# Kernel tuning notes

Hardware: AMD Instinct MI355X
Metric: run time of the kernel (lower is better)

## Reference

```python
import jax, jax.numpy as jnp
import numpy as np

N_NODES = 100000
N_EDGES = 3200000
IN_SIZE = 128
HID = 128
OUT = 64
HEADS = (4, 1)
NEG_SLOPE = 0.2  # DGL GATConv default leaky_relu slope


def setup_inputs() -> dict:
    key = jax.random.key(0)
    ks = jax.random.split(key, 10)
    x = jax.random.normal(ks[0], (N_NODES, IN_SIZE), dtype=jnp.float32)
    src = jax.random.randint(ks[1], (N_EDGES,), 0, N_NODES, dtype=jnp.int64)
    dst = jax.random.randint(ks[2], (N_EDGES,), 0, N_NODES, dtype=jnp.int64)
    s1 = 1.0 / np.sqrt(IN_SIZE)
    s2 = 1.0 / np.sqrt(HID * HEADS[0])
    W1 = jax.random.normal(ks[3], (IN_SIZE, HEADS[0] * HID), dtype=jnp.float32) * s1
    al1 = jax.random.normal(ks[4], (HEADS[0], HID), dtype=jnp.float32) * 0.1
    ar1 = jax.random.normal(ks[5], (HEADS[0], HID), dtype=jnp.float32) * 0.1
    W2 = jax.random.normal(ks[6], (HEADS[0] * HID, HEADS[1] * OUT), dtype=jnp.float32) * s2
    al2 = jax.random.normal(ks[7], (HEADS[1], OUT), dtype=jnp.float32) * 0.1
    ar2 = jax.random.normal(ks[8], (HEADS[1], OUT), dtype=jnp.float32) * 0.1
    return {"x": x, "W1": W1, "al1": al1, "ar1": ar1, "W2": W2,
            "al2": al2, "ar2": ar2, "src": src, "dst": dst}


def gat_conv(h, W, al, ar, src, dst, n_heads, d_out):
    # h: (N, F_in); W: (F_in, n_heads*d_out); al/ar: (n_heads, d_out)
    n = h.shape[0]
    feat = (h @ W).reshape(n, n_heads, d_out)          # (N, H, D)
    el = jnp.sum(feat * al, axis=-1)                    # (N, H) source score
    er = jnp.sum(feat * ar, axis=-1)                    # (N, H) dest score
    e = jax.nn.leaky_relu(el[src] + er[dst], NEG_SLOPE)  # (E, H)
    # edge softmax over incoming edges of each destination node
    m = jax.ops.segment_max(e, dst, num_segments=n)     # (N, H)
    m = jnp.where(jnp.isfinite(m), m, 0.0)              # nodes with no in-edges
    ex = jnp.exp(e - m[dst])                            # (E, H)
    s = jax.ops.segment_sum(ex, dst, num_segments=n)    # (N, H)
    alpha = ex / s[dst]                                 # (E, H); s[dst]>0 always
    msg = alpha[:, :, None] * feat[src]                 # (E, H, D)
    out = jax.ops.segment_sum(msg, dst, num_segments=n)  # (N, H, D)
    return out


def reference(x, W1, al1, ar1, W2, al2, ar2, src, dst):
    n = x.shape[0]
    h = gat_conv(x, W1, al1, ar1, src, dst, HEADS[0], HID)   # (N, H1, HID)
    h = jax.nn.elu(h).reshape(n, HEADS[0] * HID)             # flatten(1)
    h = gat_conv(h, W2, al2, ar2, src, dst, HEADS[1], OUT)   # (N, H2, OUT)
    h = h.reshape(n * HEADS[1], OUT)                          # view(N*H2, OUT)
    return h
```

## Files before the change

kernel.cpp:

```cpp
#include <hip/hip_runtime.h>
#include <math.h>

#define N_NODES 100000
#define N_EDGES 3200000
#define NEG 0.2f
#define NPB 128
#define NB  782
#define CAP 4608
#define LOG2E 1.442695041f

typedef __attribute__((ext_vector_type(8))) short short8;
typedef __attribute__((ext_vector_type(4))) float f32x4;
typedef __attribute__((ext_vector_type(2))) float f32x2;

__device__ __forceinline__ float bflo(unsigned int u){
  union { unsigned int i; float f; } v; v.i = u << 16; return v.f;
}
__device__ __forceinline__ float bfhi(unsigned int u){
  union { unsigned int i; float f; } v; v.i = u & 0xffff0000u; return v.f;
}
__device__ __forceinline__ unsigned short f2bf(float f){
  union { float f; unsigned int i; } v; v.f = f;
  unsigned int r = v.i + 0x7fffu + ((v.i >> 16) & 1u);
  return (unsigned short)(r >> 16);
}
__device__ __forceinline__ unsigned int packbf(float lo, float hi){
  return (unsigned int)f2bf(lo) | ((unsigned int)f2bf(hi) << 16);
}
__device__ __forceinline__ unsigned int pk_fp8x4(float a, float b, float c, float d){
  int v = 0;
  v = __builtin_amdgcn_cvt_pk_fp8_f32(a, b, v, false);
  v = __builtin_amdgcn_cvt_pk_fp8_f32(c, d, v, true);
  return (unsigned int)v;
}
__device__ __forceinline__ f32x2 unpk_fp8_lo(unsigned int v){
  return __builtin_amdgcn_cvt_pk_f32_fp8((int)v, false);
}
__device__ __forceinline__ f32x2 unpk_fp8_hi(unsigned int v){
  return __builtin_amdgcn_cvt_pk_f32_fp8((int)v, true);
}
__device__ __forceinline__ void pk_fma(f32x2 &acc, f32x2 a, f32x2 w){
  asm("v_pk_fma_f32 %0, %1, %2, %0" : "+v"(acc) : "v"(a), "v"(w));
}
__device__ __forceinline__ float wexp(float t){
  return __builtin_amdgcn_exp2f(fmaxf(t, NEG * t));
}
__device__ __forceinline__ void fma16(f32x2* acc, uint4 q, float w){
  f32x2 W; W[0]=w; W[1]=w;
  pk_fma(acc[0], unpk_fp8_lo(q.x), W);
  pk_fma(acc[1], unpk_fp8_hi(q.x), W);
  pk_fma(acc[2], unpk_fp8_lo(q.y), W);
  pk_fma(acc[3], unpk_fp8_hi(q.y), W);
  pk_fma(acc[4], unpk_fp8_lo(q.z), W);
  pk_fma(acc[5], unpk_fp8_hi(q.z), W);
  pk_fma(acc[6], unpk_fp8_lo(q.w), W);
  pk_fma(acc[7], unpk_fp8_hi(q.w), W);
}

__global__ void k_prep(const float* __restrict__ W1, const float* __restrict__ W2,
                       unsigned short* __restrict__ W1t, unsigned short* __restrict__ W2t,
                       int* __restrict__ bcur){
  int i = blockIdx.x*256 + threadIdx.x;
  if (i < 65536){ int n = i >> 7, k = i & 127; W1t[i] = f2bf(W1[k*512 + n]); }
  else if (i < 98304){ int j = i - 65536; int n = j >> 9, k = j & 511; W2t[j] = f2bf(W2[k*64 + n]); }
  else if (i < 98304 + NB){ int b = i - 98304; bcur[b*16] = b*CAP; }
}

__global__ __launch_bounds__(256) void k_mm1(const float* __restrict__ A,
    const unsigned short* __restrict__ Bt,
    unsigned char* __restrict__ C8, int M,
    const float* __restrict__ al, const float* __restrict__ ar,
    float* __restrict__ el, float* __restrict__ er){
  __shared__ unsigned short sm[18432];
  unsigned short* As = sm;
  unsigned short* Bs = sm + 9216;
  const int t = threadIdx.x;
  const int w = t >> 6, l = t & 63;
  const int quad = l >> 4, l16 = l & 15;
  const int m0 = blockIdx.x * 128;
  const int head = blockIdx.y;
  const int moff = (w & 1) * 64, noff = (w >> 1) * 64;
  f32x4 acc[4][4];
  #pragma unroll
  for (int i=0;i<4;++i)
    #pragma unroll
    for (int j=0;j<4;++j){ acc[i][j][0]=0.f; acc[i][j][1]=0.f; acc[i][j][2]=0.f; acc[i][j][3]=0.f; }
  for (int kb = 0; kb < 2; ++kb){
    const int K0 = kb * 64;
    #pragma unroll
    for (int i=0;i<8;++i){
      int idx = t + i*256;
      int row = idx >> 4, c4 = (idx & 15) * 4;
      float4 v = make_float4(0.f,0.f,0.f,0.f);
      if (m0 + row < M) v = *(const float4*)(A + (size_t)(m0+row)*128 + K0 + c4);
      uint2 p; p.x = packbf(v.x, v.y); p.y = packbf(v.z, v.w);
      *(uint2*)(As + row*72 + c4) = p;
    }
    #pragma unroll
    for (int i=0;i<4;++i){
      int idx = t + i*256;
      int row = idx >> 3, c8 = (idx & 7) * 8;
      *(uint4*)(Bs + row*72 + c8) =
        *(const uint4*)(Bt + (size_t)(head*128 + row)*128 + K0 + c8);
    }
    __syncthreads();
    #pragma unroll
    for (int ks = 0; ks < 2; ++ks){
      short8 af[4], bfr[4];
      #pragma unroll
      for (int mi=0; mi<4; ++mi)
        af[mi] = *(const short8*)(As + (moff + mi*16 + l16)*72 + ks*32 + quad*8);
      #pragma unroll
      for (int ni=0; ni<4; ++ni)
        bfr[ni] = *(const short8*)(Bs + (noff + ni*16 + l16)*72 + ks*32 + quad*8);
      #pragma unroll
      for (int mi=0; mi<4; ++mi)
        #pragma unroll
        for (int ni=0; ni<4; ++ni)
          acc[mi][ni] = __builtin_amdgcn_mfma_f32_16x16x32_bf16(af[mi], bfr[ni], acc[mi][ni], 0,0,0);
    }
    __syncthreads();
  }
  unsigned short* Cs = sm;
  #pragma unroll
  for (int mi=0; mi<4; ++mi)
    #pragma unroll
    for (int ni=0; ni<4; ++ni){
      int col = noff + ni*16 + l16;
      int rb  = moff + mi*16 + quad*4;
      #pragma unroll
      for (int r=0;r<4;++r) Cs[(rb+r)*136 + col] = f2bf(acc[mi][ni][r]);
    }
  __syncthreads();
  const int hcol = head * 128;
  #pragma unroll
  for (int i=0;i<8;++i){
    int e = t + i*256;
    int row = e >> 4, c8 = (e & 15) * 8;
    uint4 qb = *(const uint4*)(Cs + row*136 + c8);
    uint2 o;
    o.x = pk_fp8x4(bflo(qb.x), bfhi(qb.x), bflo(qb.y), bfhi(qb.y));
    o.y = pk_fp8x4(bflo(qb.z), bfhi(qb.z), bflo(qb.w), bfhi(qb.w));
    if (m0 + row < M)
      *(uint2*)(C8 + (size_t)(m0+row)*512 + hcol + c8) = o;
  }
  {
    int row = t >> 1, half = t & 1;
    const float* alp = al + head*128 + half*64;
    const float* arp = ar + head*128 + half*64;
    const unsigned short* cp = Cs + row*136 + half*64;
    float se = 0.f, sr = 0.f;
    #pragma unroll
    for (int i=0;i<8;++i){
      uint4 q = *(const uint4*)(cp + i*8);
      float4 a0 = *(const float4*)(alp + i*8), a1 = *(const float4*)(alp + i*8 + 4);
      float4 r0 = *(const float4*)(arp + i*8), r1 = *(const float4*)(arp + i*8 + 4);
      se += bflo(q.x)*a0.x + bfhi(q.x)*a0.y + bflo(q.y)*a0.z + bfhi(q.y)*a0.w
          + bflo(q.z)*a1.x + bfhi(q.z)*a1.y + bflo(q.w)*a1.z + bfhi(q.w)*a1.w;
      sr += bflo(q.x)*r0.x + bfhi(q.x)*r0.y + bflo(q.y)*r0.z + bfhi(q.y)*r0.w
          + bflo(q.z)*r1.x + bfhi(q.z)*r1.y + bflo(q.w)*r1.z + bfhi(q.w)*r1.w;
    }
    se += __shfl_xor(se, 1); sr += __shfl_xor(sr, 1);
    if (half == 0 && m0 + row < M){
      el[(m0+row)*4 + head] = se * LOG2E;
      er[(m0+row)*4 + head] = sr * LOG2E;
    }
  }
}

__global__ __launch_bounds__(256) void k_mm2(const unsigned short* __restrict__ A,
    const unsigned short* __restrict__ Bt,
    unsigned short* __restrict__ C, int M,
    const float* __restrict__ al, const float* __restrict__ ar,
    float* __restrict__ el, float* __restrict__ er){
  __shared__ unsigned short sm[13824];
  unsigned short* As = sm;
  unsigned short* Bs = sm + 9216;
  const int t = threadIdx.x;
  const int w = t >> 6, l = t & 63;
  const int quad = l >> 4, l16 = l & 15;
  const int m0 = blockIdx.x * 128;
  const int moff = w * 32;
  f32x4 acc[2][4];
  #pragma unroll
  for (int i=0;i<2;++i)
    #pragma unroll
    for (int j=0;j<4;++j){ acc[i][j][0]=0.f; acc[i][j][1]=0.f; acc[i][j][2]=0.f; acc[i][j][3]=0.f; }
  for (int kb = 0; kb < 8; ++kb){
    const int K0 = kb * 64;
    #pragma unroll
    for (int i=0;i<4;++i){
      int idx = t + i*256;
      int row = idx >> 3, c8 = (idx & 7) * 8;
      uint4 v; v.x=0u; v.y=0u; v.z=0u; v.w=0u;
      if (m0 + row < M) v = *(const uint4*)(A + (size_t)(m0+row)*512 + K0 + c8);
      *(uint4*)(As + row*72 + c8) = v;
    }
    #pragma unroll
    for (int i=0;i<2;++i){
      int idx = t + i*256;
      int row = idx >> 3, c8 = (idx & 7) * 8;
      *(uint4*)(Bs + row*72 + c8) = *(const uint4*)(Bt + (size_t)row*512 + K0 + c8);
    }
    __syncthreads();
    #pragma unroll
    for (int ks = 0; ks < 2; ++ks){
      short8 af[2], bfr[4];
      #pragma unroll
      for (int mi=0; mi<2; ++mi)
        af[mi] = *(const short8*)(As + (moff + mi*16 + l16)*72 + ks*32 + quad*8);
      #pragma unroll
      for (int ni=0; ni<4; ++ni)
        bfr[ni] = *(const short8*)(Bs + (ni*16 + l16)*72 + ks*32 + quad*8);
      #pragma unroll
      for (int mi=0; mi<2; ++mi)
        #pragma unroll
        for (int ni=0; ni<4; ++ni)
          acc[mi][ni] = __builtin_amdgcn_mfma_f32_16x16x32_bf16(af[mi], bfr[ni], acc[mi][ni], 0,0,0);
    }
    __syncthreads();
  }
  unsigned short* Cs = sm;
  #pragma unroll
  for (int mi=0; mi<2; ++mi)
    #pragma unroll
    for (int ni=0; ni<4; ++ni){
      int col = ni*16 + l16;
      int rb  = moff + mi*16 + quad*4;
      #pragma unroll
      for (int r=0;r<4;++r) Cs[(rb+r)*72 + col] = f2bf(acc[mi][ni][r]);
    }
  __syncthreads();
  #pragma unroll
  for (int i=0;i<4;++i){
    int e = t + i*256;
    int row = e >> 3, c8 = (e & 7) * 8;
    if (m0 + row < M)
      *(uint4*)(C + (size_t)(m0+row)*64 + c8) = *(const uint4*)(Cs + row*72 + c8);
  }
  {
    int row = t >> 1, half = t & 1;
    const float* alp = al + half*32;
    const float* arp = ar + half*32;
    const unsigned short* cp = Cs + row*72 + half*32;
    float se = 0.f, sr = 0.f;
    #pragma unroll
    for (int i=0;i<4;++i){
      uint4 q = *(const uint4*)(cp + i*8);
      float4 a0 = *(const float4*)(alp + i*8), a1 = *(const float4*)(alp + i*8 + 4);
      float4 r0 = *(const float4*)(arp + i*8), r1 = *(const float4*)(arp + i*8 + 4);
      se += bflo(q.x)*a0.x + bfhi(q.x)*a0.y + bflo(q.y)*a0.z + bfhi(q.y)*a0.w
          + bflo(q.z)*a1.x + bfhi(q.z)*a1.y + bflo(q.w)*a1.z + bfhi(q.w)*a1.w;
      sr += bflo(q.x)*r0.x + bfhi(q.x)*r0.y + bflo(q.y)*r0.z + bfhi(q.y)*r0.w
          + bflo(q.z)*r1.x + bfhi(q.z)*r1.y + bflo(q.w)*r1.z + bfhi(q.w)*r1.w;
    }
    se += __shfl_xor(se, 1); sr += __shfl_xor(sr, 1);
    if (half == 0 && m0 + row < M){
      el[m0+row] = se * LOG2E;
      er[m0+row] = sr * LOG2E;
    }
  }
}

__global__ void k_bucket(const int* __restrict__ src, const int* __restrict__ dst,
                         int* __restrict__ bcur, int* __restrict__ staged){
  int e = blockIdx.x*blockDim.x + threadIdx.x;
  if (e < N_EDGES){
    int d = dst[e];
    int b = d >> 7;
    int pos = atomicAdd(&bcur[b*16], 1);
    staged[pos] = (src[e] << 7) | (d & (NPB-1));
  }
}
__global__ __launch_bounds__(1024) void k_bscan(const int* __restrict__ bcur,
    int* __restrict__ bbase){
  __shared__ int lds[1024];
  int t = threadIdx.x;
  int v = (t < NB) ? (bcur[t*16] - t*CAP) : 0;
  lds[t] = v; __syncthreads();
  for (int off=1; off<1024; off<<=1){
    int u = (t>=off)? lds[t-off] : 0;
    __syncthreads();
    lds[t] += u;
    __syncthreads();
  }
  if (t < NB) bbase[t] = lds[t] - v;
  if (t == 0) bbase[NB] = N_EDGES;
}
__global__ __launch_bounds__(256) void k_binsort(const int* __restrict__ staged,
    const int* __restrict__ bcur, const int* __restrict__ bbase,
    int* __restrict__ csr_src, int* __restrict__ indptr){
  __shared__ int hist[NPB];
  __shared__ int scan[NPB];
  __shared__ int lcur[NPB];
  const int b = blockIdx.x, t = threadIdx.x;
  const int st0 = b*CAP;
  const int cnt = bcur[b*16] - st0;
  const int obase = bbase[b];
  if (t < NPB) hist[t] = 0;
  __syncthreads();
  for (int i = t; i < cnt; i += 256)
    atomicAdd(&hist[staged[st0 + i] & (NPB-1)], 1);
  __syncthreads();
  int v = (t < NPB) ? hist[t] : 0;
  if (t < NPB) scan[t] = v;
  __syncthreads();
  for (int off=1; off<NPB; off<<=1){
    int u = (t < NPB && t >= off) ? scan[t-off] : 0;
    __syncthreads();
    if (t < NPB) scan[t] += u;
    __syncthreads();
  }
  const int node0 = b * NPB;
  if (t < NPB){
    int ex = obase + scan[t] - v;
    lcur[t] = ex;
    if (node0 + t < N_NODES) indptr[node0 + t] = ex;
  }
  if (b == NB-1 && t == 0) indptr[N_NODES] = N_EDGES;
  __syncthreads();
  for (int i = t; i < cnt; i += 256){
    int pv = staged[st0 + i];
    int pos = atomicAdd(&lcur[pv & (NPB-1)], 1);
    csr_src[pos] = pv >> 7;
  }
}

__global__ __launch_bounds__(256) void k_agg1(const unsigned char* __restrict__ feat,
    const float* __restrict__ el, const float* __restrict__ er,
    const int* __restrict__ indptr, const int* __restrict__ csr_src,
    unsigned short* __restrict__ out){
  int wave = threadIdx.x >> 6, lane = threadIdx.x & 63;
  int n = blockIdx.x*4 + wave;
  if (n >= N_NODES) return;
  int p0 = indptr[n], p1 = indptr[n+1];
  const int half = lane >> 5, hl = lane & 31;
  const int hh = hl >> 3;
  const unsigned d0 = hl * 16u;
  const float myer = er[n*4 + hh];
  float ssum = 0.f;
  f32x2 acc[8];
  #pragma unroll
  for (int i=0;i<8;++i){ acc[i][0]=0.f; acc[i][1]=0.f; }
  int e = p0;
  for (; e + 7 < p1; e += 8){
    int s0 = csr_src[e + 0 + half];
    int s1 = csr_src[e + 2 + half];
    int s2 = csr_src[e + 4 + half];
    int s3 = csr_src[e + 6 + half];
    uint4 q0 = *(const uint4*)(feat + (((unsigned)s0) << 9) + d0);
    uint4 q1 = *(const uint4*)(feat + (((unsigned)s1) << 9) + d0);
    uint4 q2 = *(const uint4*)(feat + (((unsigned)s2) << 9) + d0);
    uint4 q3 = *(const uint4*)(feat + (((unsigned)s3) << 9) + d0);
    float t0 = el[(s0<<2) + hh] + myer;
    float t1 = el[(s1<<2) + hh] + myer;
    float t2 = el[(s2<<2) + hh] + myer;
    float t3 = el[(s3<<2) + hh] + myer;
    float w0 = wexp(t0), w1 = wexp(t1), w2 = wexp(t2), w3 = wexp(t3);
    ssum += (w0 + w1) + (w2 + w3);
    fma16(acc, q0, w0);
    fma16(acc, q1, w1);
    fma16(acc, q2, w2);
    fma16(acc, q3, w3);
  }
  for (; e < p1; e += 2){
    int idx = e + half;
    bool ok = idx < p1;
    int s = csr_src[ok ? idx : e];
    uint4 q = *(const uint4*)(feat + (((unsigned)s) << 9) + d0);
    float w = ok ? wexp(el[(s<<2) + hh] + myer) : 0.f;
    ssum += w;
    fma16(acc, q, w);
  }
  ssum += __shfl_xor(ssum, 32);
  float o16[16];
  #pragma unroll
  for (int i=0;i<8;++i){
    o16[2*i]   = acc[i][0] + __shfl_xor(acc[i][0], 32);
    o16[2*i+1] = acc[i][1] + __shfl_xor(acc[i][1], 32);
  }
  float inv = ssum > 0.f ? 1.f/ssum : 0.f;
  #pragma unroll
  for (int i=0;i<16;++i){
    float v = o16[i] * inv;
    o16[i] = v > 0.f ? v : __expf(v) - 1.f;
  }
  if (half == 0){
    unsigned short* op = out + (size_t)n*512 + hl*16;
    uint4 oa, ob;
    oa.x = packbf(o16[0], o16[1]);  oa.y = packbf(o16[2], o16[3]);
    oa.z = packbf(o16[4], o16[5]);  oa.w = packbf(o16[6], o16[7]);
    ob.x = packbf(o16[8], o16[9]);  ob.y = packbf(o16[10],o16[11]);
    ob.z = packbf(o16[12],o16[13]); ob.w = packbf(o16[14],o16[15]);
    *(uint4*)op       = oa;
    *(uint4*)(op + 8) = ob;
  }
}

__global__ __launch_bounds__(256) void k_agg2(const unsigned short* __restrict__ feat,
    const float* __restrict__ el, const float* __restrict__ er,
    const int* __restrict__ indptr, const int* __restrict__ csr_src,
    float* __restrict__ out){
  int wave = threadIdx.x >> 6, lane = threadIdx.x & 63;
  int n = blockIdx.x*4 + wave;
  if (n >= N_NODES) return;
  int p0 = indptr[n], p1 = indptr[n+1];
  float ern = er[n];
  int g = lane >> 3, ql = lane & 7;
  float s = 0.f;
  f32x2 acc[4];
  #pragma unroll
  for (int i=0;i<4;++i){ acc[i][0]=0.f; acc[i][1]=0.f; }
  int e = p0 + g;
  for (; e + 8 < p1; e += 16){
    int sa = csr_src[e], sb = csr_src[e+8];
    uint4 va = *(const uint4*)(feat + (size_t)sa*64 + ql*8);
    uint4 vb = *(const uint4*)(feat + (size_t)sb*64 + ql*8);
    float wa = wexp(el[sa] + ern);
    float wb = wexp(el[sb] + ern);
    s += wa + wb;
    f32x2 Wa; Wa[0]=wa; Wa[1]=wa;
    f32x2 Wb; Wb[0]=wb; Wb[1]=wb;
    f32x2 a;
    a[0]=bflo(va.x); a[1]=bfhi(va.x); pk_fma(acc[0], a, Wa);
    a[0]=bflo(va.y); a[1]=bfhi(va.y); pk_fma(acc[1], a, Wa);
    a[0]=bflo(va.z); a[1]=bfhi(va.z); pk_fma(acc[2], a, Wa);
    a[0]=bflo(va.w); a[1]=bfhi(va.w); pk_fma(acc[3], a, Wa);
    a[0]=bflo(vb.x); a[1]=bfhi(vb.x); pk_fma(acc[0], a, Wb);
// ... 19 lines not shown
    #pragma unroll
    for (int i=0;i<4;++i){
      acc[i][0] += __shfl_xor(acc[i][0],m);
      acc[i][1] += __shfl_xor(acc[i][1],m);
    }
  }
  float inv = s > 0.f ? 1.f/s : 0.f;
  if (g == 0){
    float* op = out + (size_t)n*64 + ql*8;
    *(float4*)op     = make_float4(acc[0][0]*inv, acc[0][1]*inv, acc[1][0]*inv, acc[1][1]*inv);
    *(float4*)(op+4) = make_float4(acc[2][0]*inv, acc[2][1]*inv, acc[3][0]*inv, acc[3][1]*inv);
  }
}

extern "C" void kernel_launch(void* const* d_in, const int* in_sizes, int n_in,
                              void* d_out, int out_size, void* d_ws, size_t ws_size,
                              hipStream_t stream){
  const float* x   = (const float*)d_in[0];
  const float* W1  = (const float*)d_in[1];
  const float* al1 = (const float*)d_in[2];
  const float* ar1 = (const float*)d_in[3];
  const float* W2  = (const float*)d_in[4];
  const float* al2 = (const float*)d_in[5];
  const float* ar2 = (const float*)d_in[6];
  const int* src   = (const int*)d_in[7];
  const int* dst   = (const int*)d_in[8];
  float* out = (float*)d_out;

  char* ws = (char*)d_ws;
  size_t off = 0;
  auto alloc = [&](size_t bytes)->char*{
    char* p = ws + off; off += (bytes + 255) & ~(size_t)255; return p;
  };
  unsigned char*  feat1 = (unsigned char*)alloc((size_t)N_NODES*512);
  unsigned short* h1    = (unsigned short*)alloc((size_t)N_NODES*512*2);
  unsigned short* feat2b = (unsigned short*)feat1;
  unsigned short* W1t = (unsigned short*)alloc(512*128*2);
  unsigned short* W2t = (unsigned short*)alloc(64*512*2);
  float* el1 = (float*)alloc((size_t)N_NODES*4*4);
  float* er1 = (float*)alloc((size_t)N_NODES*4*4);
  float* el2 = el1;
  float* er2 = er1;
  int* bcur    = (int*)alloc((size_t)NB*16*4);
  int* bbase   = (int*)alloc((size_t)(NB+1)*4);
  int* indptr  = (int*)alloc((size_t)(N_NODES+1)*4);
  int* staged  = (int*)alloc((size_t)NB*CAP*4);
  int* csr_src = (int*)alloc((size_t)N_EDGES*4);

  dim3 b256(256);
  k_prep<<<dim3(388), b256, 0, stream>>>(W1, W2, W1t, W2t, bcur);
  k_mm1<<<dim3(782, 4), b256, 0, stream>>>(x, W1t, feat1, N_NODES, al1, ar1, el1, er1);
  k_bucket<<<dim3((N_EDGES+255)/256), b256, 0, stream>>>(src, dst, bcur, staged);
  k_bscan<<<dim3(1), dim3(1024), 0, stream>>>(bcur, bbase);
  k_binsort<<<dim3(NB), b256, 0, stream>>>(staged, bcur, bbase, csr_src, indptr);
  k_agg1<<<dim3(25000), b256, 0, stream>>>(feat1, el1, er1, indptr, csr_src, h1);
  k_mm2<<<dim3(782), b256, 0, stream>>>(h1, W2t, feat2b, N_NODES, al2, ar2, el2, er2);
  k_agg2<<<dim3(25000), b256, 0, stream>>>(feat2b, el2, er2, indptr, csr_src, out);
}
```

Measured before the change: 724.4 us.

## Fuse GEMM1 with edge bucketing and binsort into two heterogeneous kernels

Merges the first-layer projection GEMM with the edge bucketing pass in one kernel (heads 0-1 interleaved with bucket blocks), then runs heads 2-3 alongside the per-bucket sort in a second kernel. The compute-bound GEMM blocks are meant to overlap the memory and atomic-bound CSR build, and removing the single-block scan kernel cuts launches. Each binsort block now recomputes its output base by summing all preceding bucket counts. The fat kernels reserve the larger shared-memory footprint for every block, which can lower occupancy for the bucketing blocks.

```diff
diff --git a/kernel.cpp b/kernel.cpp
--- a/kernel.cpp
+++ b/kernel.cpp
@@ -66,19 +66,18 @@
   else if (i < 98304 + NB){ int b = i - 98304; bcur[b*16] = b*CAP; }
 }
 
-__global__ __launch_bounds__(256) void k_mm1(const float* __restrict__ A,
-    const unsigned short* __restrict__ Bt,
+__device__ void mm1_body(char* smraw, int mtile, int head,
+    const float* __restrict__ A, const unsigned short* __restrict__ Bt,
     unsigned char* __restrict__ C8, int M,
     const float* __restrict__ al, const float* __restrict__ ar,
     float* __restrict__ el, float* __restrict__ er){
-  __shared__ unsigned short sm[18432];
+  unsigned short* sm = (unsigned short*)smraw;
   unsigned short* As = sm;
   unsigned short* Bs = sm + 9216;
   const int t = threadIdx.x;
   const int w = t >> 6, l = t & 63;
   const int quad = l >> 4, l16 = l & 15;
-  const int m0 = blockIdx.x * 128;
-  const int head = blockIdx.y;
+  const int m0 = mtile * 128;
   const int moff = (w & 1) * 64, noff = (w >> 1) * 64;
   f32x4 acc[4][4];
   #pragma unroll
@@ -165,6 +164,99 @@
       el[(m0+row)*4 + head] = se * LOG2E;
       er[(m0+row)*4 + head] = sr * LOG2E;
     }
+  }
+}
+
+__device__ void bucket_body(int eb, const int* __restrict__ src,
+    const int* __restrict__ dst, int* __restrict__ bcur, int* __restrict__ staged){
+  int e = eb*256 + threadIdx.x;
+  if (e < N_EDGES){
+    int d = dst[e];
+    int b = d >> 7;
+    int pos = atomicAdd(&bcur[b*16], 1);
+    staged[pos] = (src[e] << 7) | (d & (NPB-1));
+  }
+}
+
+__device__ void binsort_body(char* smraw, int b, const int* __restrict__ staged,
+    const int* __restrict__ bcur, int* __restrict__ csr_src, int* __restrict__ indptr){
+  int* hist = (int*)smraw;
+  int* scan = hist + 128;
+  int* lcur = scan + 128;
+  int* red  = lcur + 128;
+  const int t = threadIdx.x;
+  const int st0 = b*CAP;
+  const int cnt = bcur[b*16] - st0;
+  int part = 0;
+  for (int i = t; i < b; i += 256) part += bcur[i*16] - i*CAP;
+  red[t] = part;
+  if (t < NPB) hist[t] = 0;
+  __syncthreads();
+  for (int off = 128; off > 0; off >>= 1){
+    if (t < off) red[t] += red[t + off];
+    __syncthreads();
+  }
+  const int obase = red[0];
+  for (int i = t; i < cnt; i += 256)
+    atomicAdd(&hist[staged[st0 + i] & (NPB-1)], 1);
+  __syncthreads();
+  int v = (t < NPB) ? hist[t] : 0;
+  if (t < NPB) scan[t] = v;
+  __syncthreads();
+  for (int off=1; off<NPB; off<<=1){
+    int u = (t < NPB && t >= off) ? scan[t-off] : 0;
+    __syncthreads();
+    if (t < NPB) scan[t] += u;
+    __syncthreads();
+  }
+  const int node0 = b * NPB;
+  if (t < NPB){
+    int ex = obase + scan[t] - v;
+    lcur[t] = ex;
+    if (node0 + t < N_NODES) indptr[node0 + t] = ex;
+  }
+  if (b == NB-1 && t == 0) indptr[N_NODES] = N_EDGES;
+  __syncthreads();
+  for (int i = t; i < cnt; i += 256){
+    int pv = staged[st0 + i];
+    int pos = atomicAdd(&lcur[pv & (NPB-1)], 1);
+    csr_src[pos] = pv >> 7;
+  }
+}
+
+__global__ __launch_bounds__(256) void k_fatA(const float* __restrict__ x,
+    const unsigned short* __restrict__ W1t, unsigned char* __restrict__ feat1,
+    const float* __restrict__ al1, const float* __restrict__ ar1,
+    float* __restrict__ el1, float* __restrict__ er1,
+    const int* __restrict__ src, const int* __restrict__ dst,
+    int* __restrict__ bcur, int* __restrict__ staged){
+  __shared__ char smraw[36864];
+  int b = blockIdx.x;
+  int r = b % 9;
+  if (r == 0){
+    int id = b / 9;
+    mm1_body(smraw, id % 782, id / 782, x, W1t, feat1, N_NODES, al1, ar1, el1, er1);
+  } else {
+    int id = (b/9)*8 + (r-1);
+    if (id < 12500) bucket_body(id, src, dst, bcur, staged);
+  }
+}
+
+__global__ __launch_bounds__(256) void k_fatB(const float* __restrict__ x,
+    const unsigned short* __restrict__ W1t, unsigned char* __restrict__ feat1,
+    const float* __restrict__ al1, const float* __restrict__ ar1,
+    float* __restrict__ el1, float* __restrict__ er1,
+    const int* __restrict__ staged, const int* __restrict__ bcur,
+    int* __restrict__ csr_src, int* __restrict__ indptr){
+  __shared__ char smraw[36864];
+  int b = blockIdx.x;
+  int r = b % 3;
+  if (r < 2){
+    int id = (b/3)*2 + r;
+    mm1_body(smraw, id % 782, 2 + id / 782, x, W1t, feat1, N_NODES, al1, ar1, el1, er1);
+  } else {
+    int id = b / 3;
+    binsort_body(smraw, id, staged, bcur, csr_src, indptr);
   }
 }
 
@@ -259,70 +351,6 @@
       el[m0+row] = se * LOG2E;
       er[m0+row] = sr * LOG2E;
     }
-  }
-}
-
-__global__ void k_bucket(const int* __restrict__ src, const int* __restrict__ dst,
-                         int* __restrict__ bcur, int* __restrict__ staged){
-  int e = blockIdx.x*blockDim.x + threadIdx.x;
-  if (e < N_EDGES){
-    int d = dst[e];
-    int b = d >> 7;
-    int pos = atomicAdd(&bcur[b*16], 1);
-    staged[pos] = (src[e] << 7) | (d & (NPB-1));
-  }
-}
-__global__ __launch_bounds__(1024) void k_bscan(const int* __restrict__ bcur,
-    int* __restrict__ bbase){
-  __shared__ int lds[1024];
-  int t = threadIdx.x;
-  int v = (t < NB) ? (bcur[t*16] - t*CAP) : 0;
-  lds[t] = v; __syncthreads();
-  for (int off=1; off<1024; off<<=1){
-    int u = (t>=off)? lds[t-off] : 0;
-    __syncthreads();
-    lds[t] += u;
-    __syncthreads();
-  }
-  if (t < NB) bbase[t] = lds[t] - v;
-  if (t == 0) bbase[NB] = N_EDGES;
-}
-__global__ __launch_bounds__(256) void k_binsort(const int* __restrict__ staged,
-    const int* __restrict__ bcur, const int* __restrict__ bbase,
-    int* __restrict__ csr_src, int* __restrict__ indptr){
-  __shared__ int hist[NPB];
-  __shared__ int scan[NPB];
-  __shared__ int lcur[NPB];
-  const int b = blockIdx.x, t = threadIdx.x;
-  const int st0 = b*CAP;
-  const int cnt = bcur[b*16] - st0;
-  const int obase = bbase[b];
-  if (t < NPB) hist[t] = 0;
-  __syncthreads();
-  for (int i = t; i < cnt; i += 256)
-    atomicAdd(&hist[staged[st0 + i] & (NPB-1)], 1);
-  __syncthreads();
-  int v = (t < NPB) ? hist[t] : 0;
-  if (t < NPB) scan[t] = v;
-  __syncthreads();
-  for (int off=1; off<NPB; off<<=1){
-    int u = (t < NPB && t >= off) ? scan[t-off] : 0;
-    __syncthreads();
-    if (t < NPB) scan[t] += u;
-    __syncthreads();
-  }
-  const int node0 = b * NPB;
-  if (t < NPB){
-    int ex = obase + scan[t] - v;
-    lcur[t] = ex;
-    if (node0 + t < N_NODES) indptr[node0 + t] = ex;
-  }
-  if (b == NB-1 && t == 0) indptr[N_NODES] = N_EDGES;
-  __syncthreads();
-  for (int i = t; i < cnt; i += 256){
-    int pv = staged[st0 + i];
-    int pos = atomicAdd(&lcur[pv & (NPB-1)], 1);
-    csr_src[pos] = pv >> 7;
   }
 }
 
@@ -489,17 +517,16 @@
   float* el2 = el1;
   float* er2 = er1;
   int* bcur    = (int*)alloc((size_t)NB*16*4);
-  int* bbase   = (int*)alloc((size_t)(NB+1)*4);
   int* indptr  = (int*)alloc((size_t)(N_NODES+1)*4);
   int* staged  = (int*)alloc((size_t)NB*CAP*4);
   int* csr_src = (int*)alloc((size_t)N_EDGES*4);
 
   dim3 b256(256);
   k_prep<<<dim3(388), b256, 0, stream>>>(W1, W2, W1t, W2t, bcur);
-  k_mm1<<<dim3(782, 4), b256, 0, stream>>>(x, W1t, feat1, N_NODES, al1, ar1, el1, er1);
-  k_bucket<<<dim3((N_EDGES+255)/256), b256, 0, stream>>>(src, dst, bcur, staged);
-  k_bscan<<<dim3(1), dim3(1024), 0, stream>>>(bcur, bbase);
-  k_binsort<<<dim3(NB), b256, 0, stream>>>(staged, bcur, bbase, csr_src, indptr);
+  k_fatA<<<dim3(14076), b256, 0, stream>>>(x, W1t, feat1, al1, ar1, el1, er1,
+                                           src, dst, bcur, staged);
+  k_fatB<<<dim3(2346), b256, 0, stream>>>(x, W1t, feat1, al1, ar1, el1, er1,
+                                          staged, bcur, csr_src, indptr);
   k_agg1<<<dim3(25000), b256, 0, stream>>>(feat1, el1, er1, indptr, csr_src, h1);
   k_mm2<<<dim3(782), b256, 0, stream>>>(h1, W2t, feat2b, N_NODES, al2, ar2, el2, er2);
   k_agg2<<<dim3(25000), b256, 0, stream>>>(feat2b, el2, er2, indptr, csr_src, out);
```

After: 780.4 us. 7.7% more time.

## Aggregate raw input features before layer-1 projection, folding attention vectors into W1

Applied to the files above, without the earlier changes.

Layer 1 now gathers neighbours' 128-wide bf16 input rows instead of 512-wide fp8 projected features. The projection by W1 moves after aggregation, with the softmax normalisation and ELU applied in a new GEMM epilogue. Attention scores are computed directly from x using W1·al and W1·ar precomputed in the prep kernel. This cuts per-edge gather bytes and drops the fp8 quantisation, at the cost of a separate conversion pass, an extra bf16 intermediate round-trip, and doing the 4-head weighted accumulation per edge in registers.

```diff
diff --git a/kernel.cpp b/kernel.cpp
--- a/kernel.cpp
+++ b/kernel.cpp
@@ -27,238 +27,92 @@
 __device__ __forceinline__ unsigned int packbf(float lo, float hi){
   return (unsigned int)f2bf(lo) | ((unsigned int)f2bf(hi) << 16);
 }
-__device__ __forceinline__ unsigned int pk_fp8x4(float a, float b, float c, float d){
-  int v = 0;
-  v = __builtin_amdgcn_cvt_pk_fp8_f32(a, b, v, false);
-  v = __builtin_amdgcn_cvt_pk_fp8_f32(c, d, v, true);
-  return (unsigned int)v;
-}
-__device__ __forceinline__ f32x2 unpk_fp8_lo(unsigned int v){
-  return __builtin_amdgcn_cvt_pk_f32_fp8((int)v, false);
-}
-__device__ __forceinline__ f32x2 unpk_fp8_hi(unsigned int v){
-  return __builtin_amdgcn_cvt_pk_f32_fp8((int)v, true);
-}
 __device__ __forceinline__ void pk_fma(f32x2 &acc, f32x2 a, f32x2 w){
   asm("v_pk_fma_f32 %0, %1, %2, %0" : "+v"(acc) : "v"(a), "v"(w));
 }
 __device__ __forceinline__ float wexp(float t){
   return __builtin_amdgcn_exp2f(fmaxf(t, NEG * t));
 }
-__device__ __forceinline__ void fma16(f32x2* acc, uint4 q, float w){
-  f32x2 W; W[0]=w; W[1]=w;
-  pk_fma(acc[0], unpk_fp8_lo(q.x), W);
-  pk_fma(acc[1], unpk_fp8_hi(q.x), W);
-  pk_fma(acc[2], unpk_fp8_lo(q.y), W);
-  pk_fma(acc[3], unpk_fp8_hi(q.y), W);
-  pk_fma(acc[4], unpk_fp8_lo(q.z), W);
-  pk_fma(acc[5], unpk_fp8_hi(q.z), W);
-  pk_fma(acc[6], unpk_fp8_lo(q.w), W);
-  pk_fma(acc[7], unpk_fp8_hi(q.w), W);
+__device__ __forceinline__ f32x4 wexp4(f32x4 t){
+  f32x4 r; r[0]=wexp(t[0]); r[1]=wexp(t[1]); r[2]=wexp(t[2]); r[3]=wexp(t[3]);
+  return r;
+}
+__device__ __forceinline__ void fma_x8(f32x2 (*acc)[4], uint4 q, f32x4 w){
+  f32x2 p0,p1,p2,p3;
+  p0[0]=bflo(q.x); p0[1]=bfhi(q.x);
+  p1[0]=bflo(q.y); p1[1]=bfhi(q.y);
+  p2[0]=bflo(q.z); p2[1]=bfhi(q.z);
+  p3[0]=bflo(q.w); p3[1]=bfhi(q.w);
+  #pragma unroll
+  for (int h=0;h<4;++h){
+    f32x2 W; W[0]=w[h]; W[1]=w[h];
+    pk_fma(acc[h][0], p0, W);
+    pk_fma(acc[h][1], p1, W);
+    pk_fma(acc[h][2], p2, W);
+    pk_fma(acc[h][3], p3, W);
+  }
 }
 
 __global__ void k_prep(const float* __restrict__ W1, const float* __restrict__ W2,
+                       const float* __restrict__ al1, const float* __restrict__ ar1,
                        unsigned short* __restrict__ W1t, unsigned short* __restrict__ W2t,
-                       int* __restrict__ bcur){
+                       int* __restrict__ bcur, float* __restrict__ val,
+                       float* __restrict__ var){
   int i = blockIdx.x*256 + threadIdx.x;
   if (i < 65536){ int n = i >> 7, k = i & 127; W1t[i] = f2bf(W1[k*512 + n]); }
   else if (i < 98304){ int j = i - 65536; int n = j >> 9, k = j & 511; W2t[j] = f2bf(W2[k*64 + n]); }
   else if (i < 98304 + NB){ int b = i - 98304; bcur[b*16] = b*CAP; }
-}
-
-__global__ __launch_bounds__(256) void k_mm1(const float* __restrict__ A,
-    const unsigned short* __restrict__ Bt,
-    unsigned char* __restrict__ C8, int M,
-    const float* __restrict__ al, const float* __restrict__ ar,
-    float* __restrict__ el, float* __restrict__ er){
-  __shared__ unsigned short sm[18432];
-  unsigned short* As = sm;
-  unsigned short* Bs = sm + 9216;
-  const int t = threadIdx.x;
-  const int w = t >> 6, l = t & 63;
-  const int quad = l >> 4, l16 = l & 15;
-  const int m0 = blockIdx.x * 128;
-  const int head = blockIdx.y;
-  const int moff = (w & 1) * 64, noff = (w >> 1) * 64;
-  f32x4 acc[4][4];
-  #pragma unroll
-  for (int i=0;i<4;++i)
-    #pragma unroll
-    for (int j=0;j<4;++j){ acc[i][j][0]=0.f; acc[i][j][1]=0.f; acc[i][j][2]=0.f; acc[i][j][3]=0.f; }
-  for (int kb = 0; kb < 2; ++kb){
-    const int K0 = kb * 64;
-    #pragma unroll
-    for (int i=0;i<8;++i){
-      int idx = t + i*256;
-      int row = idx >> 4, c4 = (idx & 15) * 4;
-      float4 v = make_float4(0.f,0.f,0.f,0.f);
-      if (m0 + row < M) v = *(const float4*)(A + (size_t)(m0+row)*128 + K0 + c4);
-      uint2 p; p.x = packbf(v.x, v.y); p.y = packbf(v.z, v.w);
-      *(uint2*)(As + row*72 + c4) = p;
-    }
-    #pragma unroll
-    for (int i=0;i<4;++i){
-      int idx = t + i*256;
-      int row = idx >> 3, c8 = (idx & 7) * 8;
-      *(uint4*)(Bs + row*72 + c8) =
-        *(const uint4*)(Bt + (size_t)(head*128 + row)*128 + K0 + c8);
-    }
-    __syncthreads();
-    #pragma unroll
-    for (int ks = 0; ks < 2; ++ks){
-      short8 af[4], bfr[4];
-      #pragma unroll
-      for (int mi=0; mi<4; ++mi)
-        af[mi] = *(const short8*)(As + (moff + mi*16 + l16)*72 + ks*32 + quad*8);
-      #pragma unroll
-      for (int ni=0; ni<4; ++ni)
-        bfr[ni] = *(const short8*)(Bs + (noff + ni*16 + l16)*72 + ks*32 + quad*8);
-      #pragma unroll
-      for (int mi=0; mi<4; ++mi)
-        #pragma unroll
-        for (int ni=0; ni<4; ++ni)
-          acc[mi][ni] = __builtin_amdgcn_mfma_f32_16x16x32_bf16(af[mi], bfr[ni], acc[mi][ni], 0,0,0);
-    }
-    __syncthreads();
-  }
-  unsigned short* Cs = sm;
-  #pragma unroll
-  for (int mi=0; mi<4; ++mi)
-    #pragma unroll
-    for (int ni=0; ni<4; ++ni){
-      int col = noff + ni*16 + l16;
-      int rb  = moff + mi*16 + quad*4;
-      #pragma unroll
-      for (int r=0;r<4;++r) Cs[(rb+r)*136 + col] = f2bf(acc[mi][ni][r]);
-    }
-  __syncthreads();
-  const int hcol = head * 128;
-  #pragma unroll
-  for (int i=0;i<8;++i){
-    int e = t + i*256;
-    int row = e >> 4, c8 = (e & 15) * 8;
-    uint4 qb = *(const uint4*)(Cs + row*136 + c8);
-    uint2 o;
-    o.x = pk_fp8x4(bflo(qb.x), bfhi(qb.x), bflo(qb.y), bfhi(qb.y));
-    o.y = pk_fp8x4(bflo(qb.z), bfhi(qb.z), bflo(qb.w), bfhi(qb.w));
-    if (m0 + row < M)
-      *(uint2*)(C8 + (size_t)(m0+row)*512 + hcol + c8) = o;
-  }
-  {
-    int row = t >> 1, half = t & 1;
-    const float* alp = al + head*128 + half*64;
-    const float* arp = ar + head*128 + half*64;
-    const unsigned short* cp = Cs + row*136 + half*64;
-    float se = 0.f, sr = 0.f;
-    #pragma unroll
-    for (int i=0;i<8;++i){
-      uint4 q = *(const uint4*)(cp + i*8);
-      float4 a0 = *(const float4*)(alp + i*8), a1 = *(const float4*)(alp + i*8 + 4);
-      float4 r0 = *(const float4*)(arp + i*8), r1 = *(const float4*)(arp + i*8 + 4);
-      se += bflo(q.x)*a0.x + bfhi(q.x)*a0.y + bflo(q.y)*a0.z + bfhi(q.y)*a0.w
-          + bflo(q.z)*a1.x + bfhi(q.z)*a1.y + bflo(q.w)*a1.z + bfhi(q.w)*a1.w;
-      sr += bflo(q.x)*r0.x + bfhi(q.x)*r0.y + bflo(q.y)*r0.z + bfhi(q.y)*r0.w
-          + bflo(q.z)*r1.x + bfhi(q.z)*r1.y + bflo(q.w)*r1.z + bfhi(q.w)*r1.w;
-    }
-    se += __shfl_xor(se, 1); sr += __shfl_xor(sr, 1);
-    if (half == 0 && m0 + row < M){
-      el[(m0+row)*4 + head] = se * LOG2E;
-      er[(m0+row)*4 + head] = sr * LOG2E;
-    }
-  }
-}
-
-__global__ __launch_bounds__(256) void k_mm2(const unsigned short* __restrict__ A,
-    const unsigned short* __restrict__ Bt,
-    unsigned short* __restrict__ C, int M,
-    const float* __restrict__ al, const float* __restrict__ ar,
-    float* __restrict__ el, float* __restrict__ er){
-  __shared__ unsigned short sm[13824];
-  unsigned short* As = sm;
-  unsigned short* Bs = sm + 9216;
-  const int t = threadIdx.x;
-  const int w = t >> 6, l = t & 63;
-  const int quad = l >> 4, l16 = l & 15;
-  const int m0 = blockIdx.x * 128;
-  const int moff = w * 32;
-  f32x4 acc[2][4];
-  #pragma unroll
-  for (int i=0;i<2;++i)
-    #pragma unroll
-    for (int j=0;j<4;++j){ acc[i][j][0]=0.f; acc[i][j][1]=0.f; acc[i][j][2]=0.f; acc[i][j][3]=0.f; }
-  for (int kb = 0; kb < 8; ++kb){
-    const int K0 = kb * 64;
-    #pragma unroll
-    for (int i=0;i<4;++i){
-      int idx = t + i*256;
-      int row = idx >> 3, c8 = (idx & 7) * 8;
-      uint4 v; v.x=0u; v.y=0u; v.z=0u; v.w=0u;
-      if (m0 + row < M) v = *(const uint4*)(A + (size_t)(m0+row)*512 + K0 + c8);
-      *(uint4*)(As + row*72 + c8) = v;
-    }
-    #pragma unroll
-    for (int i=0;i<2;++i){
-      int idx = t + i*256;
-      int row = idx >> 3, c8 = (idx & 7) * 8;
-      *(uint4*)(Bs + row*72 + c8) = *(const uint4*)(Bt + (size_t)row*512 + K0 + c8);
-    }
-    __syncthreads();
-    #pragma unroll
-    for (int ks = 0; ks < 2; ++ks){
-      short8 af[2], bfr[4];
-      #pragma unroll
-      for (int mi=0; mi<2; ++mi)
-        af[mi] = *(const short8*)(As + (moff + mi*16 + l16)*72 + ks*32 + quad*8);
-      #pragma unroll
-      for (int ni=0; ni<4; ++ni)
-        bfr[ni] = *(const short8*)(Bs + (ni*16 + l16)*72 + ks*32 + quad*8);
-      #pragma unroll
-      for (int mi=0; mi<2; ++mi)
-        #pragma unroll
-        for (int ni=0; ni<4; ++ni)
-          acc[mi][ni] = __builtin_amdgcn_mfma_f32_16x16x32_bf16(af[mi], bfr[ni], acc[mi][ni], 0,0,0);
-    }
-    __syncthreads();
-  }
-  unsigned short* Cs = sm;
-  #pragma unroll
-  for (int mi=0; mi<2; ++mi)
-    #pragma unroll
-    for (int ni=0; ni<4; ++ni){
-      int col = ni*16 + l16;
-      int rb  = moff + mi*16 + quad*4;
-      #pragma unroll
-      for (int r=0;r<4;++r) Cs[(rb+r)*72 + col] = f2bf(acc[mi][ni][r]);
-    }
-  __syncthreads();
-  #pragma unroll
-  for (int i=0;i<4;++i){
-    int e = t + i*256;
-    int row = e >> 3, c8 = (e & 7) * 8;
-    if (m0 + row < M)
-      *(uint4*)(C + (size_t)(m0+row)*64 + c8) = *(const uint4*)(Cs + row*72 + c8);
-  }
-  {
-    int row = t >> 1, half = t & 1;
-    const float* alp = al + half*32;
-    const float* arp = ar + half*32;
-    const unsigned short* cp = Cs + row*72 + half*32;
-    float se = 0.f, sr = 0.f;
-    #pragma unroll
-    for (int i=0;i<4;++i){
-      uint4 q = *(const uint4*)(cp + i*8);
-      float4 a0 = *(const float4*)(alp + i*8), a1 = *(const float4*)(alp + i*8 + 4);
-      float4 r0 = *(const float4*)(arp + i*8), r1 = *(const float4*)(arp + i*8 + 4);
-      se += bflo(q.x)*a0.x + bfhi(q.x)*a0.y + bflo(q.y)*a0.z + bfhi(q.y)*a0.w
-          + bflo(q.z)*a1.x + bfhi(q.z)*a1.y + bflo(q.w)*a1.z + bfhi(q.w)*a1.w;
-      sr += bflo(q.x)*r0.x + bfhi(q.x)*r0.y + bflo(q.y)*r0.z + bfhi(q.y)*r0.w
-          + bflo(q.z)*r1.x + bfhi(q.z)*r1.y + bflo(q.w)*r1.z + bfhi(q.w)*r1.w;
-    }
-    se += __shfl_xor(se, 1); sr += __shfl_xor(sr, 1);
-    if (half == 0 && m0 + row < M){
-      el[m0+row] = se * LOG2E;
-      er[m0+row] = sr * LOG2E;
-    }
+  else if (i >= 99328 && i < 99840){
+    int j = i - 99328; int k = j >> 2, h = j & 3;
+    float s = 0.f;
+    for (int d=0; d<128; ++d) s += W1[k*512 + h*128 + d] * al1[h*128 + d];
+    val[j] = s;
+  } else if (i >= 99840 && i < 100352){
+    int j = i - 99840; int k = j >> 2, h = j & 3;
+    float s = 0.f;
+    for (int d=0; d<128; ++d) s += W1[k*512 + h*128 + d] * ar1[h*128 + d];
+    var[j] = s;
+  }
+}
+
+__global__ __launch_bounds__(256) void k_xcvt(const float* __restrict__ x,
+    const float* __restrict__ val, const float* __restrict__ var,
+    unsigned short* __restrict__ xb, float* __restrict__ el, float* __restrict__ er){
+  int wave = threadIdx.x >> 6, lane = threadIdx.x & 63;
+  int q = lane >> 4, ql = lane & 15;
+  int n = (blockIdx.x*4 + wave)*4 + q;
+  f32x4 valr[8], varr[8];
+  #pragma unroll
+  for (int j=0;j<8;++j){
+    valr[j] = *(const f32x4*)(val + (ql*8+j)*4);
+    varr[j] = *(const f32x4*)(var + (ql*8+j)*4);
+  }
+  const float* xp = x + (size_t)n*128 + ql*8;
+  float4 xa = *(const float4*)xp;
+  float4 xc = *(const float4*)(xp + 4);
+  uint4 o; o.x = packbf(xa.x,xa.y); o.y = packbf(xa.z,xa.w);
+  o.z = packbf(xc.x,xc.y); o.w = packbf(xc.z,xc.w);
+  *(uint4*)(xb + (size_t)n*128 + ql*8) = o;
+  float xs[8] = {xa.x,xa.y,xa.z,xa.w,xc.x,xc.y,xc.z,xc.w};
+  f32x4 e4; e4[0]=0.f; e4[1]=0.f; e4[2]=0.f; e4[3]=0.f;
+  f32x4 r4 = e4;
+  #pragma unroll
+  for (int j=0;j<8;++j){
+    e4 += valr[j] * xs[j];
+    r4 += varr[j] * xs[j];
+  }
+  #pragma unroll
+  for (int m=1;m<16;m<<=1){
+    #pragma unroll
+    for (int c=0;c<4;++c){
+      e4[c] += __shfl_xor(e4[c], m);
+      r4[c] += __shfl_xor(r4[c], m);
+    }
+  }
+  if (ql == 0){
+    f32x4 es = e4 * LOG2E, rs = r4 * LOG2E;
+    *(f32x4*)(el + n*4) = es;
+    *(f32x4*)(er + n*4) = rs;
   }
 }
 
@@ -326,74 +180,261 @@
   }
 }
 
-__global__ __launch_bounds__(256) void k_agg1(const unsigned char* __restrict__ feat,
+__global__ __launch_bounds__(256) void k_agg1(const unsigned short* __restrict__ xb,
     const float* __restrict__ el, const float* __restrict__ er,
     const int* __restrict__ indptr, const int* __restrict__ csr_src,
-    unsigned short* __restrict__ out){
+    unsigned short* __restrict__ sagg, float* __restrict__ ssumA){
   int wave = threadIdx.x >> 6, lane = threadIdx.x & 63;
   int n = blockIdx.x*4 + wave;
   if (n >= N_NODES) return;
   int p0 = indptr[n], p1 = indptr[n+1];
-  const int half = lane >> 5, hl = lane & 31;
-  const int hh = hl >> 3;
-  const unsigned d0 = hl * 16u;
-  const float myer = er[n*4 + hh];
-  float ssum = 0.f;
-  f32x2 acc[8];
-  #pragma unroll
-  for (int i=0;i<8;++i){ acc[i][0]=0.f; acc[i][1]=0.f; }
+  const int q = lane >> 4, ql = lane & 15;
+  f32x4 er4 = *(const f32x4*)(er + n*4);
+  f32x4 ss; ss[0]=0.f; ss[1]=0.f; ss[2]=0.f; ss[3]=0.f;
+  f32x2 acc[4][4];
+  #pragma unroll
+  for (int h=0;h<4;++h)
+    #pragma unroll
+    for (int j=0;j<4;++j){ acc[h][j][0]=0.f; acc[h][j][1]=0.f; }
   int e = p0;
-  for (; e + 7 < p1; e += 8){
-    int s0 = csr_src[e + 0 + half];
-    int s1 = csr_src[e + 2 + half];
-    int s2 = csr_src[e + 4 + half];
-    int s3 = csr_src[e + 6 + half];
-    uint4 q0 = *(const uint4*)(feat + (((unsigned)s0) << 9) + d0);
-    uint4 q1 = *(const uint4*)(feat + (((unsigned)s1) << 9) + d0);
-    uint4 q2 = *(const uint4*)(feat + (((unsigned)s2) << 9) + d0);
-    uint4 q3 = *(const uint4*)(feat + (((unsigned)s3) << 9) + d0);
-    float t0 = el[(s0<<2) + hh] + myer;
-    float t1 = el[(s1<<2) + hh] + myer;
-    float t2 = el[(s2<<2) + hh] + myer;
-    float t3 = el[(s3<<2) + hh] + myer;
-    float w0 = wexp(t0), w1 = wexp(t1), w2 = wexp(t2), w3 = wexp(t3);
-    ssum += (w0 + w1) + (w2 + w3);
-    fma16(acc, q0, w0);
-    fma16(acc, q1, w1);
-    fma16(acc, q2, w2);
-    fma16(acc, q3, w3);
-  }
-  for (; e < p1; e += 2){
-    int idx = e + half;
+  for (; e + 15 < p1; e += 16){
+    int s0 = csr_src[e + 0  + q];
+    int s1 = csr_src[e + 4  + q];
+    int s2 = csr_src[e + 8  + q];
+    int s3 = csr_src[e + 12 + q];
+    uint4 q0 = *(const uint4*)(xb + (size_t)s0*128 + ql*8);
+    uint4 q1 = *(const uint4*)(xb + (size_t)s1*128 + ql*8);
+    uint4 q2 = *(const uint4*)(xb + (size_t)s2*128 + ql*8);
+    uint4 q3 = *(const uint4*)(xb + (size_t)s3*128 + ql*8);
+    f32x4 e0 = *(const f32x4*)(el + s0*4);
+    f32x4 e1 = *(const f32x4*)(el + s1*4);
+    f32x4 e2 = *(const f32x4*)(el + s2*4);
+    f32x4 e3 = *(const f32x4*)(el + s3*4);
+    f32x4 w0 = wexp4(e0 + er4);
+    f32x4 w1 = wexp4(e1 + er4);
+    f32x4 w2 = wexp4(e2 + er4);
+    f32x4 w3 = wexp4(e3 + er4);
+    ss += (w0 + w1) + (w2 + w3);
+    fma_x8(acc, q0, w0);
+    fma_x8(acc, q1, w1);
+    fma_x8(acc, q2, w2);
+    fma_x8(acc, q3, w3);
+  }
+  for (; e < p1; e += 4){
+    int idx = e + q;
     bool ok = idx < p1;
     int s = csr_src[ok ? idx : e];
-    uint4 q = *(const uint4*)(feat + (((unsigned)s) << 9) + d0);
-    float w = ok ? wexp(el[(s<<2) + hh] + myer) : 0.f;
-    ssum += w;
-    fma16(acc, q, w);
-  }
-  ssum += __shfl_xor(ssum, 32);
-  float o16[16];
+    uint4 qq = *(const uint4*)(xb + (size_t)s*128 + ql*8);
+    f32x4 ee = *(const f32x4*)(el + s*4);
+    f32x4 w = wexp4(ee + er4);
+    if (!ok){ w[0]=0.f; w[1]=0.f; w[2]=0.f; w[3]=0.f; }
+    ss += w;
+    fma_x8(acc, qq, w);
+  }
+  #pragma unroll
+  for (int m=16;m<64;m<<=1){
+    #pragma unroll
+    for (int c=0;c<4;++c) ss[c] += __shfl_xor(ss[c], m);
+    #pragma unroll
+    for (int h=0;h<4;++h)
+      #pragma unroll
+      for (int j=0;j<4;++j){
+        acc[h][j][0] += __shfl_xor(acc[h][j][0], m);
+        acc[h][j][1] += __shfl_xor(acc[h][j][1], m);
+      }
+  }
+  if (q == 0){
+    unsigned short* op = sagg + (size_t)n*512 + ql*8;
+    #pragma unroll
+    for (int h=0;h<4;++h){
+      uint4 o;
+      o.x = packbf(acc[h][0][0], acc[h][0][1]);
+      o.y = packbf(acc[h][1][0], acc[h][1][1]);
+      o.z = packbf(acc[h][2][0], acc[h][2][1]);
+      o.w = packbf(acc[h][3][0], acc[h][3][1]);
+      *(uint4*)(op + h*128) = o;
+    }
+    if (ql == 0) *(f32x4*)(ssumA + n*4) = ss;
+  }
+}
+
+__global__ __launch_bounds__(256) void k_mmpost(unsigned short* __restrict__ sagg,
+    const unsigned short* __restrict__ Bt, const float* __restrict__ ssumA, int M){
+  __shared__ unsigned short sm[18432];
+  unsigned short* As = sm;
+  unsigned short* Bs = sm + 9216;
+  const int t = threadIdx.x;
+  const int w = t >> 6, l = t & 63;
+  const int quad = l >> 4, l16 = l & 15;
+  const int m0 = blockIdx.x * 128;
+  const int h = blockIdx.y;
+  const int moff = (w & 1) * 64, noff = (w >> 1) * 64;
+  f32x4 acc[4][4];
+  #pragma unroll
+  for (int i=0;i<4;++i)
+    #pragma unroll
+    for (int j=0;j<4;++j){ acc[i][j][0]=0.f; acc[i][j][1]=0.f; acc[i][j][2]=0.f; acc[i][j][3]=0.f; }
+  for (int kb = 0; kb < 2; ++kb){
+    const int K0 = kb * 64;
+    #pragma unroll
+    for (int i=0;i<4;++i){
+      int idx = t + i*256;
+      int row = idx >> 3, c8 = (idx & 7) * 8;
+      uint4 v; v.x=0u; v.y=0u; v.z=0u; v.w=0u;
+      if (m0 + row < M)
+        v = *(const uint4*)(sagg + (size_t)(m0+row)*512 + h*128 + K0 + c8);
+      *(uint4*)(As + row*72 + c8) = v;
+    }
+    #pragma unroll
+    for (int i=0;i<4;++i){
+      int idx = t + i*256;
+      int row = idx >> 3, c8 = (idx & 7) * 8;
+      *(uint4*)(Bs + row*72 + c8) =
+        *(const uint4*)(Bt + (size_t)(h*128 + row)*128 + K0 + c8);
+    }
+    __syncthreads();
+    #pragma unroll
+    for (int ks = 0; ks < 2; ++ks){
+      short8 af[4], bfr[4];
+      #pragma unroll
+      for (int mi=0; mi<4; ++mi)
+        af[mi] = *(const short8*)(As + (moff + mi*16 + l16)*72 + ks*32 + quad*8);
+      #pragma unroll
+      for (int ni=0; ni<4; ++ni)
+        bfr[ni] = *(const short8*)(Bs + (noff + ni*16 + l16)*72 + ks*32 + quad*8);
+      #pragma unroll
+      for (int mi=0; mi<4; ++mi)
+        #pragma unroll
+        for (int ni=0; ni<4; ++ni)
+          acc[mi][ni] = __builtin_amdgcn_mfma_f32_16x16x32_bf16(af[mi], bfr[ni], acc[mi][ni], 0,0,0);
+    }
+    __syncthreads();
+  }
+  float invr[4][4];
+  #pragma unroll
+  for (int mi=0; mi<4; ++mi)
+    #pragma unroll
+    for (int r=0;r<4;++r){
+      int gr = m0 + moff + mi*16 + quad*4 + r;
+      float s = (gr < M) ? ssumA[gr*4 + h] : 0.f;
+      invr[mi][r] = s > 0.f ? 1.f/s : 0.f;
+    }
+  unsigned short* Cs = sm;
+  #pragma unroll
+  for (int mi=0; mi<4; ++mi)
+    #pragma unroll
+    for (int ni=0; ni<4; ++ni){
+      int col = noff + ni*16 + l16;
+      int rb  = moff + mi*16 + quad*4;
+      #pragma unroll
+      for (int r=0;r<4;++r){
+        float v = acc[mi][ni][r] * invr[mi][r];
+        v = v > 0.f ? v : __expf(v) - 1.f;
+        Cs[(rb+r)*136 + col] = f2bf(v);
+      }
+    }
+  __syncthreads();
   #pragma unroll
   for (int i=0;i<8;++i){
-    o16[2*i]   = acc[i][0] + __shfl_xor(acc[i][0], 32);
-    o16[2*i+1] = acc[i][1] + __shfl_xor(acc[i][1], 32);
-  }
-  float inv = ssum > 0.f ? 1.f/ssum : 0.f;
-  #pragma unroll
-  for (int i=0;i<16;++i){
-    float v = o16[i] * inv;
-    o16[i] = v > 0.f ? v : __expf(v) - 1.f;
-  }
-  if (half == 0){
-    unsigned short* op = out + (size_t)n*512 + hl*16;
-    uint4 oa, ob;
-    oa.x = packbf(o16[0], o16[1]);  oa.y = packbf(o16[2], o16[3]);
-    oa.z = packbf(o16[4], o16[5]);  oa.w = packbf(o16[6], o16[7]);
-    ob.x = packbf(o16[8], o16[9]);  ob.y = packbf(o16[10],o16[11]);
-    ob.z = packbf(o16[12],o16[13]); ob.w = packbf(o16[14],o16[15]);
-    *(uint4*)op       = oa;
-    *(uint4*)(op + 8) = ob;
+    int e = t + i*256;
+    int row = e >> 4, c8 = (e & 15) * 8;
+    if (m0 + row < M)
+      *(uint4*)(sagg + (size_t)(m0+row)*512 + h*128 + c8) =
+        *(const uint4*)(Cs + row*136 + c8);
+  }
+}
+
+__global__ __launch_bounds__(256) void k_mm2(const unsigned short* __restrict__ A,
+    const unsigned short* __restrict__ Bt,
+    unsigned short* __restrict__ C, int M,
+    const float* __restrict__ al, const float* __restrict__ ar,
+    float* __restrict__ el, float* __restrict__ er){
+  __shared__ unsigned short sm[13824];
+  unsigned short* As = sm;
+  unsigned short* Bs = sm + 9216;
+  const int t = threadIdx.x;
+  const int w = t >> 6, l = t & 63;
+  const int quad = l >> 4, l16 = l & 15;
+  const int m0 = blockIdx.x * 128;
+  const int moff = w * 32;
+  f32x4 acc[2][4];
+  #pragma unroll
+  for (int i=0;i<2;++i)
+    #pragma unroll
+    for (int j=0;j<4;++j){ acc[i][j][0]=0.f; acc[i][j][1]=0.f; acc[i][j][2]=0.f; acc[i][j][3]=0.f; }
+  for (int kb = 0; kb < 8; ++kb){
+    const int K0 = kb * 64;
+    #pragma unroll
+    for (int i=0;i<4;++i){
+      int idx = t + i*256;
+      int row = idx >> 3, c8 = (idx & 7) * 8;
+      uint4 v; v.x=0u; v.y=0u; v.z=0u; v.w=0u;
+      if (m0 + row < M) v = *(const uint4*)(A + (size_t)(m0+row)*512 + K0 + c8);
+      *(uint4*)(As + row*72 + c8) = v;
+    }
+    #pragma unroll
+    for (int i=0;i<2;++i){
+      int idx = t + i*256;
+      int row = idx >> 3, c8 = (idx & 7) * 8;
+      *(uint4*)(Bs + row*72 + c8) = *(const uint4*)(Bt + (size_t)row*512 + K0 + c8);
+    }
+    __syncthreads();
+    #pragma unroll
+    for (int ks = 0; ks < 2; ++ks){
+      short8 af[2], bfr[4];
+      #pragma unroll
+      for (int mi=0; mi<2; ++mi)
+        af[mi] = *(const short8*)(As + (moff + mi*16 + l16)*72 + ks*32 + quad*8);
+      #pragma unroll
+      for (int ni=0; ni<4; ++ni)
+        bfr[ni] = *(const short8*)(Bs + (ni*16 + l16)*72 + ks*32 + quad*8);
+      #pragma unroll
+      for (int mi=0; mi<2; ++mi)
+        #pragma unroll
+        for (int ni=0; ni<4; ++ni)
+          acc[mi][ni] = __builtin_amdgcn_mfma_f32_16x16x32_bf16(af[mi], bfr[ni], acc[mi][ni], 0,0,0);
+    }
+    __syncthreads();
+  }
+  unsigned short* Cs = sm;
+  #pragma unroll
+  for (int mi=0; mi<2; ++mi)
+    #pragma unroll
+    for (int ni=0; ni<4; ++ni){
+      int col = ni*16 + l16;
+      int rb  = moff + mi*16 + quad*4;
+      #pragma unroll
+      for (int r=0;r<4;++r) Cs[(rb+r)*72 + col] = f2bf(acc[mi][ni][r]);
+    }
+  __syncthreads();
+  #pragma unroll
+  for (int i=0;i<4;++i){
+    int e = t + i*256;
+    int row = e >> 3, c8 = (e & 7) * 8;
+    if (m0 + row < M)
+      *(uint4*)(C + (size_t)(m0+row)*64 + c8) = *(const uint4*)(Cs + row*72 + c8);
+  }
+  {
+    int row = t >> 1, half = t & 1;
+    const float* alp = al + half*32;
+    const float* arp = ar + half*32;
+    const unsigned short* cp = Cs + row*72 + half*32;
+    float se = 0.f, sr = 0.f;
+    #pragma unroll
+    for (int i=0;i<4;++i){
+      uint4 q = *(const uint4*)(cp + i*8);
+      float4 a0 = *(const float4*)(alp + i*8), a1 = *(const float4*)(alp + i*8 + 4);
+      float4 r0 = *(const float4*)(arp + i*8), r1 = *(const float4*)(arp + i*8 + 4);
+      se += bflo(q.x)*a0.x + bfhi(q.x)*a0.y + bflo(q.y)*a0.z + bfhi(q.y)*a0.w
+          + bflo(q.z)*a1.x + bfhi(q.z)*a1.y + bflo(q.w)*a1.z + bfhi(q.w)*a1.w;
+      sr += bflo(q.x)*r0.x + bfhi(q.x)*r0.y + bflo(q.y)*r0.z + bfhi(q.y)*r0.w
+          + bflo(q.z)*r1.x + bfhi(q.z)*r1.y + bflo(q.w)*r1.z + bfhi(q.w)*r1.w;
+    }
+    se += __shfl_xor(se, 1); sr += __shfl_xor(sr, 1);
+    if (half == 0 && m0 + row < M){
+      el[m0+row] = se * LOG2E;
+      er[m0+row] = sr * LOG2E;
+    }
   }
 }
 
@@ -479,11 +520,13 @@
   auto alloc = [&](size_t bytes)->char*{
     char* p = ws + off; off += (bytes + 255) & ~(size_t)255; return p;
   };
-  unsigned char*  feat1 = (unsigned char*)alloc((size_t)N_NODES*512);
-  unsigned short* h1    = (unsigned short*)alloc((size_t)N_NODES*512*2);
-  unsigned short* feat2b = (unsigned short*)feat1;
+  unsigned short* xbuf = (unsigned short*)alloc((size_t)N_NODES*128*2);
+  unsigned short* sagg = (unsigned short*)alloc((size_t)N_NODES*512*2);
+  float* ssumA = (float*)alloc((size_t)N_NODES*4*4);
   unsigned short* W1t = (unsigned short*)alloc(512*128*2);
   unsigned short* W2t = (unsigned short*)alloc(64*512*2);
+  float* val  = (float*)alloc(512*4);
+  float* var  = (float*)alloc(512*4);
   float* el1 = (float*)alloc((size_t)N_NODES*4*4);
   float* er1 = (float*)alloc((size_t)N_NODES*4*4);
   float* el2 = el1;
@@ -493,14 +536,16 @@
   int* indptr  = (int*)alloc((size_t)(N_NODES+1)*4);
   int* staged  = (int*)alloc((size_t)NB*CAP*4);
   int* csr_src = (int*)alloc((size_t)N_EDGES*4);
+  unsigned short* feat2b = (unsigned short*)staged;
 
   dim3 b256(256);
-  k_prep<<<dim3(388), b256, 0, stream>>>(W1, W2, W1t, W2t, bcur);
-  k_mm1<<<dim3(782, 4), b256, 0, stream>>>(x, W1t, feat1, N_NODES, al1, ar1, el1, er1);
+  k_prep<<<dim3(392), b256, 0, stream>>>(W1, W2, al1, ar1, W1t, W2t, bcur, val, var);
+  k_xcvt<<<dim3(6250), b256, 0, stream>>>(x, val, var, xbuf, el1, er1);
   k_bucket<<<dim3((N_EDGES+255)/256), b256, 0, stream>>>(src, dst, bcur, staged);
   k_bscan<<<dim3(1), dim3(1024), 0, stream>>>(bcur, bbase);
   k_binsort<<<dim3(NB), b256, 0, stream>>>(staged, bcur, bbase, csr_src, indptr);
-  k_agg1<<<dim3(25000), b256, 0, stream>>>(feat1, el1, er1, indptr, csr_src, h1);
-  k_mm2<<<dim3(782), b256, 0, stream>>>(h1, W2t, feat2b, N_NODES, al2, ar2, el2, er2);
+  k_agg1<<<dim3(25000), b256, 0, stream>>>(xbuf, el1, er1, indptr, csr_src, sagg, ssumA);
+  k_mmpost<<<dim3(782, 4), b256, 0, stream>>>(sagg, W1t, ssumA, N_NODES);
+  k_mm2<<<dim3(782), b256, 0, stream>>>(sagg, W2t, feat2b, N_NODES, al2, ar2, el2, er2);
   k_agg2<<<dim3(25000), b256, 0, stream>>>(feat2b, el2, er2, indptr, csr_src, out);
 }
```

Measured after the change: 680.8 us. 6.0% less time.
